# Optimization experiments

Measured on AMD Instinct MI355X. Metric: run time of the kernel, lower is better.

The kernel has to match this reference:

```python
import jax, jax.numpy as jnp
import numpy as np

B, N, D = 8, 1024, 256
H = 8
DH = D // H
R = 4          # relation types 0..3; adj value 4 = no relation
FF = 1024
EPS = 1e-5


def _lin(k, fan_in, shape):
    return jax.random.normal(k, shape, jnp.float32) * (1.0 / np.sqrt(fan_in))


def setup_inputs() -> dict:
    key = jax.random.key(0)
    ks = jax.random.split(key, 16)
    src = jax.random.normal(ks[0], (B, N, D), jnp.float32)
    adj_matrix = jax.random.randint(ks[1], (B, N, N), 0, 5, dtype=jnp.int32)
    Wq = _lin(ks[2], D, (D, D)); bq = jnp.zeros((D,), jnp.float32)
    Wk = _lin(ks[3], D, (D, D)); bk = jnp.zeros((D,), jnp.float32)
    Wv = _lin(ks[4], D, (R, D, D)); bv = jnp.zeros((R, D), jnp.float32)
    Wo = _lin(ks[5], D, (D, D)); bo = jnp.zeros((D,), jnp.float32)
    W1 = _lin(ks[6], D, (D, FF)); b1 = jnp.zeros((FF,), jnp.float32)
    W2 = _lin(ks[7], FF, (FF, D)); b2 = jnp.zeros((D,), jnp.float32)
    g1 = jnp.ones((D,), jnp.float32); beta1 = jnp.zeros((D,), jnp.float32)
    g2 = jnp.ones((D,), jnp.float32); beta2 = jnp.zeros((D,), jnp.float32)
    return dict(src=src, adj_matrix=adj_matrix, Wq=Wq, bq=bq, Wk=Wk, bk=bk,
                Wv=Wv, bv=bv, Wo=Wo, bo=bo, W1=W1, b1=b1, W2=W2, b2=b2,
                g1=g1, beta1=beta1, g2=g2, beta2=beta2)


def _ln(x, g, b):
    m = x.mean(-1, keepdims=True)
    v = ((x - m) ** 2).mean(-1, keepdims=True)
    return (x - m) * jax.lax.rsqrt(v + EPS) * g + b


def reference(src, adj_matrix, Wq, bq, Wk, bk, Wv, bv, Wo, bo, W1, b1, W2, b2, g1, beta1, g2, beta2):
    Bb, Nn, Dm = src.shape
    h, dh = H, Dm // H
    q = (src @ Wq + bq).reshape(Bb, Nn, h, dh).transpose(0, 2, 1, 3)  # (B,H,N,dh)
    k = (src @ Wk + bk).reshape(Bb, Nn, h, dh).transpose(0, 2, 1, 3)
    scores = jnp.einsum('bhid,bhjd->bhij', q, k) / np.sqrt(dh)
    attn = jax.nn.softmax(scores, axis=-1)                             # (B,H,N,N)
    out = jnp.zeros_like(q)
    for r in range(Wv.shape[0]):  # small fixed relation loop, matches module
        v_r = (src @ Wv[r] + bv[r]).reshape(Bb, Nn, h, dh).transpose(0, 2, 1, 3)
        mask = (adj_matrix == r)[:, None]                              # (B,1,N,N)
        out = out + jnp.einsum('bhij,bhjd->bhid', attn * mask, v_r)
    attn_out = out.transpose(0, 2, 1, 3).reshape(Bb, Nn, Dm) @ Wo + bo
    x = _ln(src + attn_out, g1, beta1)
    ff = jax.nn.gelu(x @ W1 + b1, approximate=False) @ W2 + b2
    return _ln(x + ff, g2, beta2)
```

## Files before the change

kernel.cpp:

```cpp
#include <hip/hip_runtime.h>
#include <hip/hip_bf16.h>
#include <cmath>

constexpr int CB  = 8;
constexpr int CN  = 1024;
constexpr int CD  = 256;
constexpr int CH  = 8;
constexpr int CDH = 32;
constexpr int CR  = 4;
constexpr int CFF = 1024;
constexpr float CEPS = 1e-5f;
constexpr size_t SZH = (size_t)CB * CH * CN * CDH;

#define MODE_QK    0
#define MODE_FFN1  2
#define MODE_VT    4

typedef float v4f __attribute__((ext_vector_type(4)));
typedef short v8s __attribute__((ext_vector_type(8)));

static __device__ __forceinline__ short f2bf(float f) {
    unsigned u = __builtin_bit_cast(unsigned, f);
    u += 0x7fff + ((u >> 16) & 1);
    return (short)(u >> 16);
}
static __device__ __forceinline__ float bf2f(short s) {
    unsigned u = ((unsigned)(unsigned short)s) << 16;
    return __builtin_bit_cast(float, u);
}

static __device__ __forceinline__ void async_copy16(const void* g, void* l) {
    __builtin_amdgcn_global_load_lds(
        (const __attribute__((address_space(1))) void*)g,
        (__attribute__((address_space(3))) void*)l, 16, 0, 0);
}

template<int BM, int BN, int MODE>
__device__ __forceinline__ void gemm_body(
    const short* __restrict__ A, const short* __restrict__ Bw,
    const float* __restrict__ biasv, void* __restrict__ dest,
    int M, int K, int Nw, int bx, int by, short* smem)
{
    constexpr int WTM = BM / 2, WTN = BN / 2;
    constexpr int TM = WTM / 16, TN = WTN / 16;
    short* As = smem;
    short* Bs = smem + 2 * BM * 32;

    const int t    = threadIdx.x;
    const int lane = t & 63;
    const int w    = t >> 6;
    const int quad = lane >> 4, l15 = lane & 15;
    const int wm = w >> 1, wn = w & 1;
    const int m0 = bx * BM, n0 = by * BN;

    const int srow = lane >> 2;
    const int scol = (lane & 3) * 8;

    v4f acc[TM][TN];
    #pragma unroll
    for (int i = 0; i < TM; ++i)
        #pragma unroll
        for (int j = 0; j < TN; ++j) acc[i][j] = (v4f){0.f, 0.f, 0.f, 0.f};

    const int NK = K >> 5;

    auto stage = [&](int buf, int kt) {
        #pragma unroll
        for (int u = 0; u < BM / 64; ++u) {
            const int e0 = (w * (BM / 64) + u) * 512;
            const int row = (e0 >> 5) + srow;
            async_copy16(A + (size_t)(m0 + row) * K + kt + scol,
                         &As[buf * BM * 32 + e0]);
        }
        #pragma unroll
        for (int u = 0; u < BN / 64; ++u) {
            const int e0 = (w * (BN / 64) + u) * 512;
            const int row = (e0 >> 5) + srow;
            async_copy16(Bw + (size_t)(n0 + row) * K + kt + scol,
                         &Bs[buf * BN * 32 + e0]);
        }
    };

    stage(0, 0);

    for (int it = 0; it < NK; ++it) {
        __syncthreads();
        if (it + 1 < NK) stage((it + 1) & 1, (it + 1) << 5);

        const int buf = it & 1;
        v8s af[TM], bfr[TN];
        #pragma unroll
        for (int i = 0; i < TM; ++i)
            af[i] = *(const v8s*)&As[buf * BM * 32 +
                                     (wm * WTM + i * 16 + l15) * 32 + quad * 8];
        #pragma unroll
        for (int j = 0; j < TN; ++j)
            bfr[j] = *(const v8s*)&Bs[buf * BN * 32 +
                                      (wn * WTN + j * 16 + l15) * 32 + quad * 8];
        #pragma unroll
        for (int i = 0; i < TM; ++i)
            #pragma unroll
            for (int j = 0; j < TN; ++j)
                acc[i][j] = __builtin_amdgcn_mfma_f32_16x16x32_bf16(
                    af[i], bfr[j], acc[i][j], 0, 0, 0);
    }

    #pragma unroll
    for (int i = 0; i < TM; ++i) {
        #pragma unroll
        for (int j = 0; j < TN; ++j) {
            const int mb = m0 + wm * WTM + i * 16 + quad * 4;
            const int n  = n0 + wn * WTN + j * 16 + l15;
            float vals[4];
            if (MODE == MODE_VT) {
                #pragma unroll
                for (int rr = 0; rr < 4; ++rr) vals[rr] = acc[i][j][rr] + biasv[mb + rr];
            } else {
                #pragma unroll
                for (int rr = 0; rr < 4; ++rr) vals[rr] = acc[i][j][rr] + biasv[n];
            }

            if (MODE == MODE_QK) {
                const int b = mb >> 10, ii0 = mb & 1023;
                const int plane = n >> 8, nn = n & 255;
                const int h = nn >> 5, d = nn & 31;
                #pragma unroll
                for (int rr = 0; rr < 4; ++rr)
                    ((short*)dest)[(size_t)plane * SZH +
                        (((size_t)(b * CH + h)) * CN + ii0 + rr) * CDH + d] =
                        f2bf(vals[rr]);
            } else if (MODE == MODE_VT) {
                const int b = n >> 10, ii = n & 1023;
                #pragma unroll
                for (int rr = 0; rr < 4; ++rr) {
                    const int m = mb + rr;
                    const int r2 = m >> 8, hd = m & 255;
                    const int h = hd >> 5, d = hd & 31;
                    ((short*)dest)[2 * SZH +
                        (((size_t)(r2 * 64 + b * CH + h)) * CDH + d) * CN + ii] =
                        f2bf(vals[rr]);
                }
            } else {
                #pragma unroll
                for (int rr = 0; rr < 4; ++rr) {
                    const size_t idx = (size_t)(mb + rr) * Nw + n;
                    const float xx = vals[rr];
                    const float E = exp2f(2.302217f * (xx + 0.044715f * xx * xx * xx));
                    ((short*)dest)[idx] = f2bf(xx * E / (E + 1.f));
                }
            }
        }
    }
}

template<int BM, int BN, int MODE>
__global__ __launch_bounds__(256)
void gemm_mfma(const short* __restrict__ A, const short* __restrict__ Bw,
               const float* __restrict__ biasv, void* __restrict__ dest,
               int M, int K, int Nw)
{
    extern __shared__ short smem[];
    gemm_body<BM, BN, MODE>(A, Bw, biasv, dest, M, K, Nw,
                            blockIdx.x, blockIdx.y, smem);
}

__global__ __launch_bounds__(256)
void proj_kernel(const short* __restrict__ src_bf, const short* __restrict__ wqkvT,
                 const float* __restrict__ bpack, short* __restrict__ qkv,
                 const int* __restrict__ adj, unsigned char* __restrict__ adj4)
{
    extern __shared__ short smem[];
    const int g = blockIdx.x;
    if (g < 512) {
        gemm_body<64, 128, MODE_QK>(src_bf, wqkvT, bpack, qkv,
                                    8192, 256, 512, g >> 2, g & 3, smem);
    } else if (g < 1536) {
        const int h2 = g - 512;
        gemm_body<64, 128, MODE_VT>(wqkvT + 512 * 256, src_bf, bpack + 512,
                                    qkv, 1024, 256, 8192, h2 & 15, h2 >> 4, smem);
    } else {
        const int nout = CB * CN * CN / 8;
        for (int i = (g - 1536) * 256 + threadIdx.x; i < nout; i += 512 * 256) {
            const int4 a0 = ((const int4*)adj)[2 * i];
            const int4 a1 = ((const int4*)adj)[2 * i + 1];
            const unsigned p =
                (unsigned)(a0.x & 0xf)        | ((unsigned)(a0.y & 0xf) << 4)  |
                ((unsigned)(a0.z & 0xf) << 8) | ((unsigned)(a0.w & 0xf) << 12) |
                ((unsigned)(a1.x & 0xf) << 16)| ((unsigned)(a1.y & 0xf) << 20) |
                ((unsigned)(a1.z & 0xf) << 24)| ((unsigned)(a1.w & 0xf) << 28);
            ((unsigned*)adj4)[i] = p;
        }
    }
}

template<bool OUTF, bool OUTB, bool ADDBF>
__global__ __launch_bounds__(256)
void gemm_ln32(const short* __restrict__ A, const short* __restrict__ Bw,
               const float* __restrict__ biasv, const void* __restrict__ addp,
               const float* __restrict__ gw, const float* __restrict__ be,
               float* __restrict__ outf, short* __restrict__ outb, int K)
{
    __shared__ short As[2][32 * 32];
    __shared__ short Bs[2][256 * 32];
    __shared__ float redS[2][16][2], redQ[2][16][2];

    const int t    = threadIdx.x;
    const int lane = t & 63;
    const int w    = t >> 6;
    const int quad = lane >> 4, l15 = lane & 15;
    const int wr   = w >> 1;
    const int wg   = w & 1;
    const int m0   = blockIdx.x * 32;

    const int srow = lane >> 2;
    const int scol = (lane & 3) * 8;

    v4f acc[8];
    #pragma unroll
    for (int j = 0; j < 8; ++j) acc[j] = (v4f){0.f, 0.f, 0.f, 0.f};

    const int NK = K >> 5;

    auto stage = [&](int buf, int kt) {
        if (w < 2)
            async_copy16(A + (size_t)(m0 + 16 * w + srow) * K + kt + scol,
                         &As[buf][w * 512]);
        #pragma unroll
        for (int u = 0; u < 4; ++u) {
            const int e0 = (w * 4 + u) * 512;
            async_copy16(Bw + (size_t)((e0 >> 5) + srow) * K + kt + scol,
                         &Bs[buf][e0]);
        }
    };

    stage(0, 0);

    for (int it = 0; it < NK; ++it) {
        __syncthreads();
        if (it + 1 < NK) stage((it + 1) & 1, (it + 1) << 5);

        const int buf = it & 1;
        const v8s af = *(const v8s*)&As[buf][(16 * wr + l15) * 32 + quad * 8];
        #pragma unroll
        for (int j = 0; j < 8; ++j) {
            const v8s bfr = *(const v8s*)&Bs[buf][(wg * 128 + 16 * j + l15) * 32 + quad * 8];
            acc[j] = __builtin_amdgcn_mfma_f32_16x16x32_bf16(af, bfr, acc[j], 0, 0, 0);
        }
    }

    float v[4][8];
    #pragma unroll
    for (int rr = 0; rr < 4; ++rr) {
        const int row = m0 + 16 * wr + quad * 4 + rr;
        float s = 0.f, sq = 0.f;
        #pragma unroll
        for (int j = 0; j < 8; ++j) {
            const int n = wg * 128 + 16 * j + l15;
            const size_t idx = (size_t)row * CD + n;
            const float addv = ADDBF ? bf2f(((const short*)addp)[idx])
                                     : ((const float*)addp)[idx];
            const float x = acc[j][rr] + biasv[n] + addv;
            v[rr][j] = x;
            s += x; sq += x * x;
        }
        #pragma unroll
        for (int off = 1; off < 16; off <<= 1) {
            s  += __shfl_xor(s, off);
            sq += __shfl_xor(sq, off);
        }
        if (l15 == 0) {
            redS[wr][quad * 4 + rr][wg] = s;
            redQ[wr][quad * 4 + rr][wg] = sq;
        }
    }
    __syncthreads();

    #pragma unroll
    for (int rr = 0; rr < 4; ++rr) {
        const int r16 = quad * 4 + rr;
        const int row = m0 + 16 * wr + r16;
        const float s  = redS[wr][r16][0] + redS[wr][r16][1];
        const float sq = redQ[wr][r16][0] + redQ[wr][r16][1];
        const float mean = s * (1.f / CD);
        const float var  = sq * (1.f / CD) - mean * mean;
        const float rstd = rsqrtf(var + CEPS);
        #pragma unroll
        for (int j = 0; j < 8; ++j) {
            const int n = wg * 128 + 16 * j + l15;
            const float y = (v[rr][j] - mean) * rstd * gw[n] + be[n];
            if (OUTF) outf[(size_t)row * CD + n] = y;
            if (OUTB) outb[(size_t)row * CD + n] = f2bf(y);
        }
    }
}

__global__ __launch_bounds__(256)
void prep(const float* __restrict__ src,
          const float* __restrict__ Wq, const float* __restrict__ Wk,
          const float* __restrict__ Wv, const float* __restrict__ Wo,
          const float* __restrict__ W1, const float* __restrict__ W2,
          const float* __restrict__ bq, const float* __restrict__ bk,
          const float* __restrict__ bv, const float* __restrict__ bo,
          const float* __restrict__ b1, const float* __restrict__ b2,
          short* __restrict__ src_bf,
          short* __restrict__ wqkvT, short* __restrict__ woT,
          short* __restrict__ w1T, short* __restrict__ w2T,
          float* __restrict__ bpack)
{
    __shared__ float tile[64][65];
    const int bx = blockIdx.x, t = threadIdx.x;
    if (bx < 2048) {
        const int i = bx * 256 + t;
        const float4 v = ((const float4*)src)[i];
        short4 o;
        o.x = f2bf(v.x); o.y = f2bf(v.y); o.z = f2bf(v.z); o.w = f2bf(v.w);
        ((short4*)src_bf)[i] = o;
    } else if (bx < 2288) {
        const int tt = bx - 2048;
        const float* S; short* D;
        int Sstride, Dstride, k0, srccol, dstrow;
        if (tt < 96) {
            const int tk = tt & 3, tn = tt >> 2;
            const int ng = tn * 64;
            Sstride = 256; Dstride = 256; k0 = tk * 64;
            dstrow = tn * 64; D = wqkvT;
            if (ng < 256)      { S = Wq; srccol = ng; }
            else if (ng < 512) { S = Wk; srccol = ng - 256; }
            else { const int r = (ng - 512) >> 8;
                   S = Wv + (size_t)r * 65536; srccol = (ng - 512) & 255; }
        } else if (tt < 112) {
            const int u = tt - 96, tk = u & 3, tn = u >> 2;
            S = Wo; Sstride = 256; D = woT; Dstride = 256;
            k0 = tk * 64; srccol = tn * 64; dstrow = tn * 64;
        } else if (tt < 176) {
            const int u = tt - 112, tk = u & 3, tn = u >> 2;
            S = W1; Sstride = 1024; D = w1T; Dstride = 256;
            k0 = tk * 64; srccol = tn * 64; dstrow = tn * 64;
        } else {
            const int u = tt - 176, tk = u & 15, tn = u >> 4;
            S = W2; Sstride = 256; D = w2T; Dstride = 1024;
            k0 = tk * 64; srccol = tn * 64; dstrow = tn * 64;
        }
        #pragma unroll
        for (int u2 = 0; u2 < 4; ++u2) {
            const int kl = (t >> 4) + u2 * 16;
            const int nl = (t & 15) * 4;
            const float4 v = *(const float4*)&S[(size_t)(k0 + kl) * Sstride + srccol + nl];
            tile[kl][nl + 0] = v.x; tile[kl][nl + 1] = v.y;
            tile[kl][nl + 2] = v.z; tile[kl][nl + 3] = v.w;
        }
        __syncthreads();
        #pragma unroll
        for (int u2 = 0; u2 < 4; ++u2) {
            const int nl = (t >> 4) + u2 * 16;
            const int kl = (t & 15) * 4;
            short4 o;
            o.x = f2bf(tile[kl + 0][nl]); o.y = f2bf(tile[kl + 1][nl]);
            o.z = f2bf(tile[kl + 2][nl]); o.w = f2bf(tile[kl + 3][nl]);
            *(short4*)&D[(size_t)(dstrow + nl) * Dstride + k0 + kl] = o;
        }
    } else {
        const int idx = (bx - 2288) * 256 + t;
        float bvv;
        if (idx < 256)       bvv = bq[idx];
        else if (idx < 512)  bvv = bk[idx - 256];
        else if (idx < 1536) bvv = bv[idx - 512];
        else if (idx < 1792) bvv = bo[idx - 1536];
        else if (idx < 2816) bvv = b1[idx - 1792];
        else                 bvv = b2[idx - 2816];
        bpack[idx] = bvv;
    }
}

__global__ __launch_bounds__(256)
void attn_mfma(const short* __restrict__ qg, const short* __restrict__ kg,
               const short* __restrict__ vt, const unsigned char* __restrict__ adj4,
               short* __restrict__ outh)
{
    __shared__ __align__(16) short ks[2][64 * 32];
    __shared__ __align__(16) short vtile[4][32][72];
    __shared__ __align__(16) short ps[64][68];
    __shared__ __align__(16) unsigned char adjs[64][40];
    __shared__ int lut[64][4];

    const int t    = threadIdx.x;
    const int lane = t & 63;
    const int w    = t >> 6;
    const int quad = lane >> 4;
    const int l15  = lane & 15;
    const int g    = blockIdx.x;
    const int b    = g & 7;
    const int h    = (g >> 3) & 7;
    const int i0   = (g >> 6) * 64;
    const int bhh  = b * CH + h;
    const size_t bh = (size_t)bhh;

    if (t < 64) {
        const int b0 = t & 7, b1 = t >> 3;
        #pragma unroll
        for (int r = 0; r < 4; ++r) {
            const int lo = (b0 == r) ? 0x0100 : 0x0c0c;
            const int hi = (b1 == r) ? 0x0302 : 0x0c0c;
            lut[t][r] = lo | (hi << 16);
        }
    }

    const v8s qfrag = *(const v8s*)&qg[(bh * CN + i0 + 16 * w + l15) * CDH + quad * 8];

    v4f oacc[2];
    oacc[0] = (v4f){0.f, 0.f, 0.f, 0.f};
    oacc[1] = (v4f){0.f, 0.f, 0.f, 0.f};
    float plsum[4] = {0.f, 0.f, 0.f, 0.f};

    const float cs = 0.25503480f;
    const int arow = 16 * w + l15;

    const int srow = lane >> 2;
    const int scol = (lane & 3) * 8;
    const int vd0  = lane >> 3;
    const int vc   = (lane & 7) * 8;
    const short* vplane = vt + (((size_t)(w * 64 + bhh)) * CDH) * CN;
    const unsigned char* adjg =
        adj4 + ((size_t)(b * CN) + i0 + (t >> 2)) * (CN / 2) + (t & 3) * 8;

    v8s vpre[4];
    int2 apre;

    async_copy16(kg + (bh * CN + 16 * w + srow) * CDH + scol,
                 &ks[0][(16 * w + srow) * 32]);
    #pragma unroll
    for (int it = 0; it < 4; ++it)
        vpre[it] = *(const v8s*)&vplane[(size_t)(vd0 + 8 * it) * CN + vc];
    apre = *(const int2*)adjg;

    for (int jt = 0; jt < 16; ++jt) {
        __syncthreads();

        #pragma unroll
        for (int it = 0; it < 4; ++it)
            *(v8s*)&vtile[w][vd0 + 8 * it][vc] = vpre[it];
        *(int2*)&adjs[t >> 2][(t & 3) * 8] = apre;
        __syncthreads();

        if (jt + 1 < 16) {
            const int j1 = (jt + 1) * 64;
            async_copy16(kg + (bh * CN + j1 + 16 * w + srow) * CDH + scol,
                         &ks[(jt + 1) & 1][(16 * w + srow) * 32]);
            #pragma unroll
            for (int it = 0; it < 4; ++it)
                vpre[it] = *(const v8s*)&vplane[(size_t)(vd0 + 8 * it) * CN + j1 + vc];
            apre = *(const int2*)(adjg + (jt + 1) * 32);
        }

        const short* ksb = ks[jt & 1];
        v4f sacc[4];
        #pragma unroll
        for (int jb = 0; jb < 4; ++jb) {
            const v8s kfrag = *(const v8s*)&ksb[(16 * jb + l15) * 32 + quad * 8];
            sacc[jb] = __builtin_amdgcn_mfma_f32_16x16x32_bf16(
                qfrag, kfrag, (v4f){0.f, 0.f, 0.f, 0.f}, 0, 0, 0);
        }

        #pragma unroll
        for (int rr = 0; rr < 4; ++rr) {
            const int prow = 16 * w + quad * 4 + rr;
            float p[4];
            #pragma unroll
            for (int jb = 0; jb < 4; ++jb) p[jb] = exp2f(cs * sacc[jb][rr]);
            plsum[rr] += (p[0] + p[1]) + (p[2] + p[3]);
            #pragma unroll
            for (int jb = 0; jb < 4; ++jb)
                ps[prow][16 * jb + l15] = f2bf(p[jb]);
        }

        #pragma unroll
        for (int kb = 0; kb < 2; ++kb) {
            const int4 praw = *(const int4*)&ps[arow][32 * kb + quad * 8];
            const int ab32 = *(const int*)&adjs[arow][16 * kb + quad * 4];
            const int P[4] = {praw.x, praw.y, praw.z, praw.w};
            int pf[4][4];
            #pragma unroll
            for (int u = 0; u < 4; ++u) {
                const int byte = (ab32 >> (8 * u)) & 0xff;
                const int idx = (byte & 7) | ((byte >> 1) & 0x38);
                const int4 sel = *(const int4*)&lut[idx][0];
                pf[0][u] = __builtin_amdgcn_perm(P[u], P[u], sel.x);
                pf[1][u] = __builtin_amdgcn_perm(P[u], P[u], sel.y);
                pf[2][u] = __builtin_amdgcn_perm(P[u], P[u], sel.z);
                pf[3][u] = __builtin_amdgcn_perm(P[u], P[u], sel.w);
            }
            #pragma unroll
            for (int r = 0; r < 4; ++r) {
                const v8s pfr = __builtin_bit_cast(v8s,
                    make_int4(pf[r][0], pf[r][1], pf[r][2], pf[r][3]));
                #pragma unroll
                for (int cb = 0; cb < 2; ++cb) {
                    const v8s vfrag = *(const v8s*)&vtile[r][16 * cb + l15][32 * kb + quad * 8];
                    oacc[cb] = __builtin_amdgcn_mfma_f32_16x16x32_bf16(
                        pfr, vfrag, oacc[cb], 0, 0, 0);
                }
            }
        }
    }

    #pragma unroll
    for (int rr = 0; rr < 4; ++rr) {
        float l = plsum[rr];
        #pragma unroll
        for (int off = 1; off < 16; off <<= 1) l += __shfl_xor(l, off);
        const float inv = 1.f / l;
        const int row = i0 + 16 * w + quad * 4 + rr;
        #pragma unroll
        for (int cb = 0; cb < 2; ++cb)
            outh[((size_t)b * CN + row) * CD + h * CDH + 16 * cb + l15] =
                f2bf(oacc[cb][rr] * inv);
    }
}

extern "C" void kernel_launch(void* const* d_in, const int* in_sizes, int n_in,
                              void* d_out, int out_size, void* d_ws, size_t ws_size,
                              hipStream_t stream)
{
    const float* src = (const float*)d_in[0];
    const int*   adj = (const int*)d_in[1];
    const float* Wq  = (const float*)d_in[2];
    const float* bq  = (const float*)d_in[3];
    const float* Wk  = (const float*)d_in[4];
    const float* bk  = (const float*)d_in[5];
    const float* Wv  = (const float*)d_in[6];
    const float* bv  = (const float*)d_in[7];
    const float* Wo  = (const float*)d_in[8];
    const float* bo  = (const float*)d_in[9];
    const float* W1  = (const float*)d_in[10];
    const float* b1  = (const float*)d_in[11];
    const float* W2  = (const float*)d_in[12];
    const float* b2  = (const float*)d_in[13];
    const float* g1  = (const float*)d_in[14];
    const float* be1 = (const float*)d_in[15];
    const float* g2  = (const float*)d_in[16];
    const float* be2 = (const float*)d_in[17];
    float* out = (float*)d_out;

    char* wsb = (char*)d_ws;
    const size_t MB = (size_t)1 << 20;

    unsigned char* adj4 = (unsigned char*)(wsb);
    short* qkv_bf = (short*)(wsb + 8 * MB);
    short* src_bf = (short*)(wsb + 32 * MB);
    short* wqkvT  = (short*)(wsb + 36 * MB);
    short* woT    = (short*)(wsb + 36 * MB + 768 * 1024);
    short* w1T    = (short*)(wsb + 36 * MB + 896 * 1024);
    short* w2T    = (short*)(wsb + 36 * MB + 1408 * 1024);
    float* bpack  = (float*)(wsb + 36 * MB + 1920 * 1024);
    short* heads_bf = (short*)(wsb + 38 * MB);
    short* x_bf   = (short*)(wsb + 32 * MB);
    short* h1_bf  = (short*)(wsb + 16 * MB);

    const int M = CB * CN;
    dim3 blk(256);

    prep<<<dim3(2300), blk, 0, stream>>>(src, Wq, Wk, Wv, Wo, W1, W2,
        bq, bk, bv, bo, b1, b2, src_bf, wqkvT, woT, w1T, w2T, bpack);

    proj_kernel<<<dim3(2048), blk, 24576, stream>>>(
        src_bf, wqkvT, bpack, qkv_bf, adj, adj4);

    attn_mfma<<<dim3(1024), blk, 0, stream>>>(
        qkv_bf, qkv_bf + SZH, qkv_bf + 2 * SZH, adj4, heads_bf);

    gemm_ln32<false, true, false><<<dim3(M / 32), blk, 0, stream>>>(
        heads_bf, woT, bpack + 1536, src, g1, be1, nullptr, x_bf, CD);

    gemm_mfma<64, 128, MODE_FFN1><<<dim3(M / 64, CFF / 128), blk, 24576, stream>>>(
        x_bf, w1T, bpack + 1792, h1_bf, M, CD, CFF);

    gemm_ln32<true, false, true><<<dim3(M / 32), blk, 0, stream>>>(
        h1_bf, w2T, bpack + 2816, x_bf, g2, be2, out, nullptr, CFF);
}
```

Baseline: 234.7 us.

## Fold softmax scale into Q, permute V/adj layouts, shrink LN-GEMM tiles, ALU masking

Pre-scales Q by the softmax constant in the projection epilogue so the attention loop skips a multiply. V columns and the packed adjacency are permuted so each lane's P values pack contiguously, letting P be written with v_cvt_pk_bf16_f32 as one 8-byte store. The LDS lookup table for relation masking is replaced with packed 16-bit add/shift mask arithmetic. The LayerNorm-fused GEMMs move to 16-row tiles, doubling block count for occupancy at the cost of reloading the weight tile more often.

```diff
diff --git a/kernel.cpp b/kernel.cpp
--- a/kernel.cpp
+++ b/kernel.cpp
@@ -10,6 +10,7 @@
 constexpr int CR  = 4;
 constexpr int CFF = 1024;
 constexpr float CEPS = 1e-5f;
+constexpr float CS = 0.25503480f;
 constexpr size_t SZH = (size_t)CB * CH * CN * CDH;
 
 #define MODE_QK    0
@@ -27,6 +28,11 @@
 static __device__ __forceinline__ float bf2f(short s) {
     unsigned u = ((unsigned)(unsigned short)s) << 16;
     return __builtin_bit_cast(float, u);
+}
+static __device__ __forceinline__ unsigned cvtpk_bf16(float lo, float hi) {
+    unsigned r;
+    asm("v_cvt_pk_bf16_f32 %0, %1, %2" : "=v"(r) : "v"(lo), "v"(hi));
+    return r;
 }
 
 static __device__ __forceinline__ void async_copy16(const void* g, void* l) {
@@ -121,6 +127,10 @@
             }
 
             if (MODE == MODE_QK) {
+                if (n0 < 256) {
+                    #pragma unroll
+                    for (int rr = 0; rr < 4; ++rr) vals[rr] *= CS;
+                }
                 const int b = mb >> 10, ii0 = mb & 1023;
                 const int plane = n >> 8, nn = n & 255;
                 const int h = nn >> 5, d = nn & 31;
@@ -131,13 +141,14 @@
                         f2bf(vals[rr]);
             } else if (MODE == MODE_VT) {
                 const int b = n >> 10, ii = n & 1023;
+                const int iip = (ii & ~63) | ((ii & 15) << 2) | ((ii >> 4) & 3);
                 #pragma unroll
                 for (int rr = 0; rr < 4; ++rr) {
                     const int m = mb + rr;
                     const int r2 = m >> 8, hd = m & 255;
                     const int h = hd >> 5, d = hd & 31;
                     ((short*)dest)[2 * SZH +
-                        (((size_t)(r2 * 64 + b * CH + h)) * CDH + d) * CN + ii] =
+                        (((size_t)(r2 * 64 + b * CH + h)) * CDH + d) * CN + iip] =
                         f2bf(vals[rr]);
                 }
             } else {
@@ -181,14 +192,20 @@
     } else {
         const int nout = CB * CN * CN / 8;
         for (int i = (g - 1536) * 256 + threadIdx.x; i < nout; i += 512 * 256) {
-            const int4 a0 = ((const int4*)adj)[2 * i];
-            const int4 a1 = ((const int4*)adj)[2 * i + 1];
-            const unsigned p =
-                (unsigned)(a0.x & 0xf)        | ((unsigned)(a0.y & 0xf) << 4)  |
-                ((unsigned)(a0.z & 0xf) << 8) | ((unsigned)(a0.w & 0xf) << 12) |
-                ((unsigned)(a1.x & 0xf) << 16)| ((unsigned)(a1.y & 0xf) << 20) |
-                ((unsigned)(a1.z & 0xf) << 24)| ((unsigned)(a1.w & 0xf) << 28);
-            ((unsigned*)adj4)[i] = p;
+            const int m   = i & 7;
+            const int T   = (i >> 3) & 15;
+            const int row = i >> 7;
+            const int* p = adj + (size_t)row * CN + T * 64 + 2 * m;
+            const int2 q0 = *(const int2*)(p);
+            const int2 q1 = *(const int2*)(p + 16);
+            const int2 q2 = *(const int2*)(p + 32);
+            const int2 q3 = *(const int2*)(p + 48);
+            const unsigned pk =
+                (unsigned)(q0.x & 0xf)         | ((unsigned)(q1.x & 0xf) << 4)  |
+                ((unsigned)(q2.x & 0xf) << 8)  | ((unsigned)(q3.x & 0xf) << 12) |
+                ((unsigned)(q0.y & 0xf) << 16) | ((unsigned)(q1.y & 0xf) << 20) |
+                ((unsigned)(q2.y & 0xf) << 24) | ((unsigned)(q3.y & 0xf) << 28);
+            ((unsigned*)adj4)[i] = pk;
         }
     }
 }
@@ -200,31 +217,29 @@
                const float* __restrict__ gw, const float* __restrict__ be,
                float* __restrict__ outf, short* __restrict__ outb, int K)
 {
-    __shared__ short As[2][32 * 32];
+    __shared__ short As[2][16 * 32];
     __shared__ short Bs[2][256 * 32];
-    __shared__ float redS[2][16][2], redQ[2][16][2];
+    __shared__ float redS[16][4], redQ[16][4];
 
     const int t    = threadIdx.x;
     const int lane = t & 63;
     const int w    = t >> 6;
     const int quad = lane >> 4, l15 = lane & 15;
-    const int wr   = w >> 1;
-    const int wg   = w & 1;
-    const int m0   = blockIdx.x * 32;
+    const int m0   = blockIdx.x * 16;
 
     const int srow = lane >> 2;
     const int scol = (lane & 3) * 8;
 
-    v4f acc[8];
-    #pragma unroll
-    for (int j = 0; j < 8; ++j) acc[j] = (v4f){0.f, 0.f, 0.f, 0.f};
+    v4f acc[4];
+    #pragma unroll
+    for (int j = 0; j < 4; ++j) acc[j] = (v4f){0.f, 0.f, 0.f, 0.f};
 
     const int NK = K >> 5;
 
     auto stage = [&](int buf, int kt) {
-        if (w < 2)
-            async_copy16(A + (size_t)(m0 + 16 * w + srow) * K + kt + scol,
-                         &As[buf][w * 512]);
+        if (t < 64)
+            async_copy16(A + (size_t)(m0 + (t >> 2)) * K + kt + (t & 3) * 8,
+                         &As[buf][t * 8]);
         #pragma unroll
         for (int u = 0; u < 4; ++u) {
             const int e0 = (w * 4 + u) * 512;
@@ -240,22 +255,22 @@
         if (it + 1 < NK) stage((it + 1) & 1, (it + 1) << 5);
 
         const int buf = it & 1;
-        const v8s af = *(const v8s*)&As[buf][(16 * wr + l15) * 32 + quad * 8];
-        #pragma unroll
-        for (int j = 0; j < 8; ++j) {
-            const v8s bfr = *(const v8s*)&Bs[buf][(wg * 128 + 16 * j + l15) * 32 + quad * 8];
+        const v8s af = *(const v8s*)&As[buf][l15 * 32 + quad * 8];
+        #pragma unroll
+        for (int j = 0; j < 4; ++j) {
+            const v8s bfr = *(const v8s*)&Bs[buf][(w * 64 + 16 * j + l15) * 32 + quad * 8];
             acc[j] = __builtin_amdgcn_mfma_f32_16x16x32_bf16(af, bfr, acc[j], 0, 0, 0);
         }
     }
 
-    float v[4][8];
+    float v[4][4];
     #pragma unroll
     for (int rr = 0; rr < 4; ++rr) {
-        const int row = m0 + 16 * wr + quad * 4 + rr;
+        const int row = m0 + quad * 4 + rr;
         float s = 0.f, sq = 0.f;
         #pragma unroll
-        for (int j = 0; j < 8; ++j) {
-            const int n = wg * 128 + 16 * j + l15;
+        for (int j = 0; j < 4; ++j) {
+            const int n = w * 64 + 16 * j + l15;
             const size_t idx = (size_t)row * CD + n;
             const float addv = ADDBF ? bf2f(((const short*)addp)[idx])
                                      : ((const float*)addp)[idx];
@@ -269,8 +284,8 @@
             sq += __shfl_xor(sq, off);
         }
         if (l15 == 0) {
-            redS[wr][quad * 4 + rr][wg] = s;
-            redQ[wr][quad * 4 + rr][wg] = sq;
+            redS[quad * 4 + rr][w] = s;
+            redQ[quad * 4 + rr][w] = sq;
         }
     }
     __syncthreads();
@@ -278,15 +293,15 @@
     #pragma unroll
     for (int rr = 0; rr < 4; ++rr) {
         const int r16 = quad * 4 + rr;
-        const int row = m0 + 16 * wr + r16;
-        const float s  = redS[wr][r16][0] + redS[wr][r16][1];
-        const float sq = redQ[wr][r16][0] + redQ[wr][r16][1];
+        const int row = m0 + r16;
+        const float s  = (redS[r16][0] + redS[r16][1]) + (redS[r16][2] + redS[r16][3]);
+        const float sq = (redQ[r16][0] + redQ[r16][1]) + (redQ[r16][2] + redQ[r16][3]);
         const float mean = s * (1.f / CD);
         const float var  = sq * (1.f / CD) - mean * mean;
         const float rstd = rsqrtf(var + CEPS);
         #pragma unroll
-        for (int j = 0; j < 8; ++j) {
-            const int n = wg * 128 + 16 * j + l15;
+        for (int j = 0; j < 4; ++j) {
+            const int n = w * 64 + 16 * j + l15;
             const float y = (v[rr][j] - mean) * rstd * gw[n] + be[n];
             if (OUTF) outf[(size_t)row * CD + n] = y;
             if (OUTB) outb[(size_t)row * CD + n] = f2bf(y);
@@ -381,7 +396,6 @@
     __shared__ __align__(16) short vtile[4][32][72];
     __shared__ __align__(16) short ps[64][68];
     __shared__ __align__(16) unsigned char adjs[64][40];
-    __shared__ int lut[64][4];
 
     const int t    = threadIdx.x;
     const int lane = t & 63;
@@ -395,16 +409,6 @@
     const int bhh  = b * CH + h;
     const size_t bh = (size_t)bhh;
 
-    if (t < 64) {
-        const int b0 = t & 7, b1 = t >> 3;
-        #pragma unroll
-        for (int r = 0; r < 4; ++r) {
-            const int lo = (b0 == r) ? 0x0100 : 0x0c0c;
-            const int hi = (b1 == r) ? 0x0302 : 0x0c0c;
-            lut[t][r] = lo | (hi << 16);
-        }
-    }
-
     const v8s qfrag = *(const v8s*)&qg[(bh * CN + i0 + 16 * w + l15) * CDH + quad * 8];
 
     v4f oacc[2];
@@ -412,7 +416,6 @@
     oacc[1] = (v4f){0.f, 0.f, 0.f, 0.f};
     float plsum[4] = {0.f, 0.f, 0.f, 0.f};
 
-    const float cs = 0.25503480f;
     const int arow = 16 * w + l15;
 
     const int srow = lane >> 2;
@@ -466,33 +469,39 @@
             const int prow = 16 * w + quad * 4 + rr;
             float p[4];
             #pragma unroll
-            for (int jb = 0; jb < 4; ++jb) p[jb] = exp2f(cs * sacc[jb][rr]);
+            for (int jb = 0; jb < 4; ++jb) p[jb] = exp2f(sacc[jb][rr]);
             plsum[rr] += (p[0] + p[1]) + (p[2] + p[3]);
-            #pragma unroll
-            for (int jb = 0; jb < 4; ++jb)
-                ps[prow][16 * jb + l15] = f2bf(p[jb]);
+            const unsigned lo = cvtpk_bf16(p[0], p[1]);
+            const unsigned hi = cvtpk_bf16(p[2], p[3]);
+            *(uint2*)&ps[prow][4 * l15] = make_uint2(lo, hi);
         }
 
         #pragma unroll
         for (int kb = 0; kb < 2; ++kb) {
             const int4 praw = *(const int4*)&ps[arow][32 * kb + quad * 8];
-            const int ab32 = *(const int*)&adjs[arow][16 * kb + quad * 4];
-            const int P[4] = {praw.x, praw.y, praw.z, praw.w};
-            int pf[4][4];
+            const unsigned ab32 = *(const unsigned*)&adjs[arow][16 * kb + quad * 4];
+            const unsigned P[4] = {(unsigned)praw.x, (unsigned)praw.y,
+                                   (unsigned)praw.z, (unsigned)praw.w};
+            unsigned pf[4][4];
             #pragma unroll
             for (int u = 0; u < 4; ++u) {
-                const int byte = (ab32 >> (8 * u)) & 0xff;
-                const int idx = (byte & 7) | ((byte >> 1) & 0x38);
-                const int4 sel = *(const int4*)&lut[idx][0];
-                pf[0][u] = __builtin_amdgcn_perm(P[u], P[u], sel.x);
-                pf[1][u] = __builtin_amdgcn_perm(P[u], P[u], sel.y);
-                pf[2][u] = __builtin_amdgcn_perm(P[u], P[u], sel.z);
-                pf[3][u] = __builtin_amdgcn_perm(P[u], P[u], sel.w);
+                const unsigned sel = 0x0c000c00u | (unsigned)u | ((unsigned)u << 16);
+                const unsigned a2 = __builtin_amdgcn_perm(ab32, ab32, sel) & 0x00F0000Fu;
+                #pragma unroll
+                for (int r = 0; r < 4; ++r) {
+                    const unsigned x = a2 ^ ((unsigned)r | ((unsigned)r << 20));
+                    unsigned tt, mm;
+                    asm("v_pk_add_i16 %0, %1, %2"
+                        : "=v"(tt) : "v"(x), "v"(0xffffffffu));
+                    asm("v_pk_ashrrev_i16 %0, %1, %2"
+                        : "=v"(mm) : "v"(0x000f000fu), "v"(tt));
+                    pf[r][u] = P[u] & mm;
+                }
             }
             #pragma unroll
             for (int r = 0; r < 4; ++r) {
                 const v8s pfr = __builtin_bit_cast(v8s,
-                    make_int4(pf[r][0], pf[r][1], pf[r][2], pf[r][3]));
+                    make_uint4(pf[r][0], pf[r][1], pf[r][2], pf[r][3]));
                 #pragma unroll
                 for (int cb = 0; cb < 2; ++cb) {
                     const v8s vfrag = *(const v8s*)&vtile[r][16 * cb + l15][32 * kb + quad * 8];
@@ -568,12 +577,12 @@
     attn_mfma<<<dim3(1024), blk, 0, stream>>>(
         qkv_bf, qkv_bf + SZH, qkv_bf + 2 * SZH, adj4, heads_bf);
 
-    gemm_ln32<false, true, false><<<dim3(M / 32), blk, 0, stream>>>(
+    gemm_ln32<false, true, false><<<dim3(M / 16), blk, 0, stream>>>(
         heads_bf, woT, bpack + 1536, src, g1, be1, nullptr, x_bf, CD);
 
     gemm_mfma<64, 128, MODE_FFN1><<<dim3(M / 64, CFF / 128), blk, 24576, stream>>>(
         x_bf, w1T, bpack + 1792, h1_bf, M, CD, CFF);
 
-    gemm_ln32<true, false, true><<<dim3(M / 32), blk, 0, stream>>>(
+    gemm_ln32<true, false, true><<<dim3(M / 16), blk, 0, stream>>>(
         h1_bf, w2T, bpack + 2816, x_bf, g2, be2, out, nullptr, CFF);
 }
```

Result: no change. 230.3 us (-1.9%).
